# Performance work log

Hardware: AMD Instinct MI355X
Metric: run time of the kernel (lower is better)

Reference implementation:

```python
import jax, jax.numpy as jnp
import numpy as np

B, N, E, ENT, D, H, L = 64, 2048, 32768, 100000, 256, 256, 512


def setup_inputs() -> dict:
    key = jax.random.key(0)
    ks = jax.random.split(key, 12)
    return {
        "neighbors": jax.random.randint(ks[0], (B, N), 0, ENT),
        "adj_row": jax.random.randint(ks[1], (B, E), 0, N),
        "adj_col": jax.random.randint(ks[2], (B, E), 0, N),
        "adj_val": jax.random.uniform(ks[3], (B, E), dtype=jnp.float32),
        "emb_table": jax.random.normal(ks[4], (ENT, D), dtype=jnp.float32),
        "W1": jax.random.normal(ks[5], (D, H), dtype=jnp.float32) * (1.0 / np.sqrt(H)),
        "b1": jax.random.normal(ks[6], (H,), dtype=jnp.float32) * 0.01,
        "W2": jax.random.normal(ks[7], (H, H), dtype=jnp.float32) * (1.0 / np.sqrt(H)),
        "b2": jax.random.normal(ks[8], (H,), dtype=jnp.float32) * 0.01,
        "fc1_w": jax.random.normal(ks[9], (H, H), dtype=jnp.float32) * (1.0 / np.sqrt(H)),
        "fc1_b": jax.random.normal(ks[10], (H,), dtype=jnp.float32) * 0.01,
        "cur_len": L,
    }


def _gcn_layer(x, W, b, adj_row, adj_col, adj_val):
    # x: [B,N,din] -> support: [B,N,dout]
    support = jnp.einsum("bnd,dh->bnh", x, W)
    # sparse adj @ support: gather columns, scale by edge value, scatter-add to rows
    gathered = jnp.take_along_axis(support, adj_col[:, :, None], axis=1)  # [B,E,h]
    weighted = gathered * adj_val[:, :, None]
    agg = jax.vmap(lambda r, g: jax.ops.segment_sum(g, r, num_segments=N))(adj_row, weighted)
    return agg + b


def reference(neighbors, adj_row, adj_col, adj_val, emb_table, W1, b1, W2, b2, fc1_w, fc1_b, cur_len):
    x = emb_table[neighbors]                                   # [B,N,D] embedding gather
    x = _gcn_layer(x, W1, b1, adj_row, adj_col, adj_val)       # GCN layer 1
    x = _gcn_layer(x, W2, b2, adj_row, adj_col, adj_val)       # GCN layer 2
    seq = x[:, :cur_len, :]                                    # keep cur_node prefix, padded to common L
    pooled = jnp.mean(seq, axis=1, keepdims=True)              # self.seq == 'mean'
    return jax.nn.relu(jnp.einsum("blh,ho->blo", pooled, fc1_w) + fc1_b)  # [B,1,H]
```

## Files before the change

kernel.cpp:

```cpp
#include <hip/hip_runtime.h>

#define B 64
#define N 2048
#define E 32768
#define D 256
#define H 256
#define CH 32
#define SEG 16
#define EPB (E / SEG)

__global__ __launch_bounds__(256) void edge_w_kernel(
    const int* __restrict__ adj_row, const int* __restrict__ adj_col,
    const float* __restrict__ adj_val, const int* __restrict__ cur_len,
    float* __restrict__ w_out, float* __restrict__ sw_out)
{
    __shared__ float wloc[N];
    __shared__ float sred[4];
    const int b = blockIdx.x, seg = blockIdx.y, tid = threadIdx.x;
    const int L = *cur_len;

    for (int i = tid; i < N; i += 256) wloc[i] = 0.f;
    __syncthreads();

    const int base = b * E + seg * EPB;
    float svp = 0.f;
    for (int e = tid; e < EPB; e += 256) {
        int r = adj_row[base + e];
        if (r < L) {
            float v = adj_val[base + e];
            atomicAdd(&wloc[adj_col[base + e]], v);
            svp += v;
        }
    }
    __syncthreads();

    for (int i = tid; i < N; i += 256) {
        float v = wloc[i];
        if (v != 0.f) atomicAdd(&w_out[(size_t)b * N + i], v);
    }
    for (int off = 32; off; off >>= 1) svp += __shfl_down(svp, off, 64);
    if ((tid & 63) == 0) sred[tid >> 6] = svp;
    __syncthreads();
    if (tid == 0) atomicAdd(&sw_out[b], sred[0] + sred[1] + sred[2] + sred[3]);
}

__global__ __launch_bounds__(256) void edge_z_kernel(
    const int* __restrict__ adj_row, const int* __restrict__ adj_col,
    const float* __restrict__ adj_val, const float* __restrict__ w,
    float* __restrict__ z_out)
{
    __shared__ float zloc[N];
    const int b = blockIdx.x, seg = blockIdx.y, tid = threadIdx.x;

    for (int i = tid; i < N; i += 256) zloc[i] = 0.f;
    __syncthreads();

    const int base = b * E + seg * EPB;
    const float* wb = w + (size_t)b * N;
    for (int e = tid; e < EPB; e += 256) {
        float wv = wb[adj_row[base + e]];
        if (wv != 0.f) atomicAdd(&zloc[adj_col[base + e]], wv * adj_val[base + e]);
    }
    __syncthreads();

    for (int i = tid; i < N; i += 256) {
        float v = zloc[i];
        if (v != 0.f) atomicAdd(&z_out[(size_t)b * N + i], v);
    }
}

__global__ __launch_bounds__(256) void gather_kernel(
    const int* __restrict__ neighbors, const float* __restrict__ emb,
    const float* __restrict__ z, float* __restrict__ u_part)
{
    const int b = blockIdx.x, chunk = blockIdx.y, tid = threadIdx.x;
    const int lane = tid & 63, rg = tid >> 6;
    const float4* __restrict__ emb4 = (const float4*)emb;
    float4 acc = make_float4(0.f, 0.f, 0.f, 0.f);

    const int n0 = chunk * (N / CH);
    #pragma unroll 4
    for (int i = 0; i < (N / CH) / 4; ++i) {
        const int n = n0 + 4 * i + rg;
        const float zv = z[(size_t)b * N + n];
        const long idx = (long)neighbors[(size_t)b * N + n];
        const float4 v = emb4[idx * (D / 4) + lane];
        acc.x += zv * v.x; acc.y += zv * v.y;
        acc.z += zv * v.z; acc.w += zv * v.w;
    }

    __shared__ float4 red[256];
    red[tid] = acc;
    __syncthreads();
    if (tid < 64) {
        float4 a = red[tid], bb = red[tid + 64], c = red[tid + 128], d = red[tid + 192];
        float4 s = make_float4(a.x + bb.x + c.x + d.x, a.y + bb.y + c.y + d.y,
                               a.z + bb.z + c.z + d.z, a.w + bb.w + c.w + d.w);
        ((float4*)u_part)[((size_t)b * CH + chunk) * (D / 4) + tid] = s;
    }
}

__global__ __launch_bounds__(256) void head_kernel(
    const float* __restrict__ u_part, const float* __restrict__ sw,
    const float* __restrict__ W1, const float* __restrict__ b1,
    const float* __restrict__ W2, const float* __restrict__ b2,
    const float* __restrict__ fc1_w, const float* __restrict__ fc1_b,
    const int* __restrict__ cur_len, float* __restrict__ out)
{
    const int b = blockIdx.x, t = threadIdx.x;
    __shared__ float su[D];
    __shared__ float sy[H];
    __shared__ float sp[H];

    float uacc = 0.f;
    #pragma unroll 8
    for (int c = 0; c < CH; ++c) uacc += u_part[((size_t)b * CH + c) * D + t];
    su[t] = uacc;
    __syncthreads();

    float acc = sw[b] * b1[t];
    #pragma unroll 8
    for (int d = 0; d < D; ++d) acc += su[d] * W1[d * H + t];
    sy[t] = acc;
    __syncthreads();

    const float invL = 1.f / (float)(*cur_len);
    acc = 0.f;
    #pragma unroll 8
    for (int k = 0; k < H; ++k) acc += sy[k] * W2[k * H + t];
    sp[t] = acc * invL + b2[t];
    __syncthreads();

    acc = fc1_b[t];
    #pragma unroll 8
    for (int k = 0; k < H; ++k) acc += sp[k] * fc1_w[k * H + t];
    out[b * H + t] = fmaxf(acc, 0.f);
}

extern "C" void kernel_launch(void* const* d_in, const int* in_sizes, int n_in,
                              void* d_out, int out_size, void* d_ws, size_t ws_size,
                              hipStream_t stream) {
    const int*   neighbors = (const int*)  d_in[0];
    const int*   adj_row   = (const int*)  d_in[1];
    const int*   adj_col   = (const int*)  d_in[2];
    const float* adj_val   = (const float*)d_in[3];
    const float* emb_table = (const float*)d_in[4];
    const float* W1        = (const float*)d_in[5];
    const float* b1        = (const float*)d_in[6];
    const float* W2        = (const float*)d_in[7];
    const float* b2        = (const float*)d_in[8];
    const float* fc1_w     = (const float*)d_in[9];
    const float* fc1_b     = (const float*)d_in[10];
    const int*   cur_len   = (const int*)  d_in[11];
    float*       out       = (float*)d_out;

    float* w_ws  = (float*)d_ws;
    float* z_ws  = w_ws + (size_t)B * N;
    float* sw_ws = z_ws + (size_t)B * N;
    float* u_ws  = sw_ws + 64;

    hipMemsetAsync(d_ws, 0, ((size_t)2 * B * N + 64) * sizeof(float), stream);

    edge_w_kernel<<<dim3(B, SEG), 256, 0, stream>>>(adj_row, adj_col, adj_val,
                                                    cur_len, w_ws, sw_ws);
    edge_z_kernel<<<dim3(B, SEG), 256, 0, stream>>>(adj_row, adj_col, adj_val,
                                                    w_ws, z_ws);
    gather_kernel<<<dim3(B, CH), 256, 0, stream>>>(neighbors, emb_table, z_ws, u_ws);
    head_kernel<<<B, 256, 0, stream>>>(u_ws, sw_ws, W1, b1, W2, b2,
                                       fc1_w, fc1_b, cur_len, out);
}
```

Baseline: 275.2 us.

## Widen edge kernels to 512 threads, split-K head kernel, dual accumulators in gather

The edge kernels now use 8 segments of 512 threads with fully unrolled edge loops instead of 16 segments of 256. This halves the shared-to-global flush atomics and exposes more independent loads per thread. The head kernel uses 1024 threads and splits each 256-wide reduction into four partial sums combined through shared memory, so each thread's serial matvec chain is a quarter as long. The gather kernel alternates between two accumulators to break the FMA dependency chain. Risks include fewer blocks per batch reducing parallelism and more barriers in the head kernel.

```diff
diff --git a/kernel.cpp b/kernel.cpp
--- a/kernel.cpp
+++ b/kernel.cpp
@@ -6,45 +6,53 @@
 #define D 256
 #define H 256
 #define CH 32
-#define SEG 16
+#define SEG 8
 #define EPB (E / SEG)
 
-__global__ __launch_bounds__(256) void edge_w_kernel(
+__global__ __launch_bounds__(512) void edge_w_kernel(
     const int* __restrict__ adj_row, const int* __restrict__ adj_col,
     const float* __restrict__ adj_val, const int* __restrict__ cur_len,
     float* __restrict__ w_out, float* __restrict__ sw_out)
 {
     __shared__ float wloc[N];
-    __shared__ float sred[4];
+    __shared__ float sred[8];
     const int b = blockIdx.x, seg = blockIdx.y, tid = threadIdx.x;
     const int L = *cur_len;
 
-    for (int i = tid; i < N; i += 256) wloc[i] = 0.f;
+    for (int i = tid; i < N; i += 512) wloc[i] = 0.f;
     __syncthreads();
 
     const int base = b * E + seg * EPB;
     float svp = 0.f;
-    for (int e = tid; e < EPB; e += 256) {
-        int r = adj_row[base + e];
+    #pragma unroll
+    for (int k = 0; k < EPB / 512; ++k) {
+        const int e = base + tid + k * 512;
+        const int r = adj_row[e];
         if (r < L) {
-            float v = adj_val[base + e];
-            atomicAdd(&wloc[adj_col[base + e]], v);
+            const float v = adj_val[e];
+            atomicAdd(&wloc[adj_col[e]], v);
             svp += v;
         }
     }
     __syncthreads();
 
-    for (int i = tid; i < N; i += 256) {
-        float v = wloc[i];
+    #pragma unroll
+    for (int i = tid; i < N; i += 512) {
+        const float v = wloc[i];
         if (v != 0.f) atomicAdd(&w_out[(size_t)b * N + i], v);
     }
     for (int off = 32; off; off >>= 1) svp += __shfl_down(svp, off, 64);
     if ((tid & 63) == 0) sred[tid >> 6] = svp;
     __syncthreads();
-    if (tid == 0) atomicAdd(&sw_out[b], sred[0] + sred[1] + sred[2] + sred[3]);
-}
-
-__global__ __launch_bounds__(256) void edge_z_kernel(
+    if (tid == 0) {
+        float s = 0.f;
+        #pragma unroll
+        for (int i = 0; i < 8; ++i) s += sred[i];
+        atomicAdd(&sw_out[b], s);
+    }
+}
+
+__global__ __launch_bounds__(512) void edge_z_kernel(
     const int* __restrict__ adj_row, const int* __restrict__ adj_col,
     const float* __restrict__ adj_val, const float* __restrict__ w,
     float* __restrict__ z_out)
@@ -52,19 +60,22 @@
     __shared__ float zloc[N];
     const int b = blockIdx.x, seg = blockIdx.y, tid = threadIdx.x;
 
-    for (int i = tid; i < N; i += 256) zloc[i] = 0.f;
+    for (int i = tid; i < N; i += 512) zloc[i] = 0.f;
     __syncthreads();
 
     const int base = b * E + seg * EPB;
-    const float* wb = w + (size_t)b * N;
-    for (int e = tid; e < EPB; e += 256) {
-        float wv = wb[adj_row[base + e]];
-        if (wv != 0.f) atomicAdd(&zloc[adj_col[base + e]], wv * adj_val[base + e]);
-    }
-    __syncthreads();
-
-    for (int i = tid; i < N; i += 256) {
-        float v = zloc[i];
+    const float* __restrict__ wb = w + (size_t)b * N;
+    #pragma unroll
+    for (int k = 0; k < EPB / 512; ++k) {
+        const int e = base + tid + k * 512;
+        const float wv = wb[adj_row[e]];
+        if (wv != 0.f) atomicAdd(&zloc[adj_col[e]], wv * adj_val[e]);
+    }
+    __syncthreads();
+
+    #pragma unroll
+    for (int i = tid; i < N; i += 512) {
+        const float v = zloc[i];
         if (v != 0.f) atomicAdd(&z_out[(size_t)b * N + i], v);
     }
 }
@@ -76,18 +87,26 @@
     const int b = blockIdx.x, chunk = blockIdx.y, tid = threadIdx.x;
     const int lane = tid & 63, rg = tid >> 6;
     const float4* __restrict__ emb4 = (const float4*)emb;
-    float4 acc = make_float4(0.f, 0.f, 0.f, 0.f);
+    float4 acc0 = make_float4(0.f, 0.f, 0.f, 0.f);
+    float4 acc1 = make_float4(0.f, 0.f, 0.f, 0.f);
 
     const int n0 = chunk * (N / CH);
-    #pragma unroll 4
+    #pragma unroll 8
     for (int i = 0; i < (N / CH) / 4; ++i) {
         const int n = n0 + 4 * i + rg;
         const float zv = z[(size_t)b * N + n];
         const long idx = (long)neighbors[(size_t)b * N + n];
         const float4 v = emb4[idx * (D / 4) + lane];
-        acc.x += zv * v.x; acc.y += zv * v.y;
-        acc.z += zv * v.z; acc.w += zv * v.w;
-    }
+        if (i & 1) {
+            acc1.x += zv * v.x; acc1.y += zv * v.y;
+            acc1.z += zv * v.z; acc1.w += zv * v.w;
+        } else {
+            acc0.x += zv * v.x; acc0.y += zv * v.y;
+            acc0.z += zv * v.z; acc0.w += zv * v.w;
+        }
+    }
+    float4 acc = make_float4(acc0.x + acc1.x, acc0.y + acc1.y,
+                             acc0.z + acc1.z, acc0.w + acc1.w);
 
     __shared__ float4 red[256];
     red[tid] = acc;
@@ -100,41 +119,66 @@
     }
 }
 
-__global__ __launch_bounds__(256) void head_kernel(
+__global__ __launch_bounds__(1024) void head_kernel(
     const float* __restrict__ u_part, const float* __restrict__ sw,
     const float* __restrict__ W1, const float* __restrict__ b1,
     const float* __restrict__ W2, const float* __restrict__ b2,
     const float* __restrict__ fc1_w, const float* __restrict__ fc1_b,
     const int* __restrict__ cur_len, float* __restrict__ out)
 {
-    const int b = blockIdx.x, t = threadIdx.x;
+    const int b = blockIdx.x;
+    const int t = threadIdx.x & 255;
+    const int s = threadIdx.x >> 8;
+    __shared__ float red[4][256];
     __shared__ float su[D];
     __shared__ float sy[H];
     __shared__ float sp[H];
 
-    float uacc = 0.f;
-    #pragma unroll 8
-    for (int c = 0; c < CH; ++c) uacc += u_part[((size_t)b * CH + c) * D + t];
-    su[t] = uacc;
-    __syncthreads();
-
-    float acc = sw[b] * b1[t];
-    #pragma unroll 8
-    for (int d = 0; d < D; ++d) acc += su[d] * W1[d * H + t];
-    sy[t] = acc;
+    float part = 0.f;
+    #pragma unroll
+    for (int c = 0; c < 8; ++c)
+        part += u_part[((size_t)b * CH + s * 8 + c) * D + t];
+    red[s][t] = part;
+    __syncthreads();
+    if (s == 0) su[t] = red[0][t] + red[1][t] + red[2][t] + red[3][t];
+    __syncthreads();
+
+    part = 0.f;
+    #pragma unroll 8
+    for (int k = 0; k < 64; ++k) {
+        const int d = s * 64 + k;
+        part += su[d] * W1[d * H + t];
+    }
+    red[s][t] = part;
+    __syncthreads();
+    if (s == 0) sy[t] = red[0][t] + red[1][t] + red[2][t] + red[3][t] + sw[b] * b1[t];
     __syncthreads();
 
     const float invL = 1.f / (float)(*cur_len);
-    acc = 0.f;
-    #pragma unroll 8
-    for (int k = 0; k < H; ++k) acc += sy[k] * W2[k * H + t];
-    sp[t] = acc * invL + b2[t];
-    __syncthreads();
-
-    acc = fc1_b[t];
-    #pragma unroll 8
-    for (int k = 0; k < H; ++k) acc += sp[k] * fc1_w[k * H + t];
-    out[b * H + t] = fmaxf(acc, 0.f);
+    part = 0.f;
+    #pragma unroll 8
+    for (int k = 0; k < 64; ++k) {
+        const int d = s * 64 + k;
+        part += sy[d] * W2[d * H + t];
+    }
+    red[s][t] = part;
+    __syncthreads();
+    if (s == 0)
+        sp[t] = (red[0][t] + red[1][t] + red[2][t] + red[3][t]) * invL + b2[t];
+    __syncthreads();
+
+    part = 0.f;
+    #pragma unroll 8
+    for (int k = 0; k < 64; ++k) {
+        const int d = s * 64 + k;
+        part += sp[d] * fc1_w[d * H + t];
+    }
+    red[s][t] = part;
+    __syncthreads();
+    if (s == 0) {
+        const float v = red[0][t] + red[1][t] + red[2][t] + red[3][t] + fc1_b[t];
+        out[(size_t)b * H + t] = fmaxf(v, 0.f);
+    }
 }
 
 extern "C" void kernel_launch(void* const* d_in, const int* in_sizes, int n_in,
@@ -161,11 +205,11 @@
 
     hipMemsetAsync(d_ws, 0, ((size_t)2 * B * N + 64) * sizeof(float), stream);
 
-    edge_w_kernel<<<dim3(B, SEG), 256, 0, stream>>>(adj_row, adj_col, adj_val,
+    edge_w_kernel<<<dim3(B, SEG), 512, 0, stream>>>(adj_row, adj_col, adj_val,
                                                     cur_len, w_ws, sw_ws);
-    edge_z_kernel<<<dim3(B, SEG), 256, 0, stream>>>(adj_row, adj_col, adj_val,
+    edge_z_kernel<<<dim3(B, SEG), 512, 0, stream>>>(adj_row, adj_col, adj_val,
                                                     w_ws, z_ws);
     gather_kernel<<<dim3(B, CH), 256, 0, stream>>>(neighbors, emb_table, z_ws, u_ws);
-    head_kernel<<<B, 256, 0, stream>>>(u_ws, sw_ws, W1, b1, W2, b2,
-                                       fc1_w, fc1_b, cur_len, out);
-}
+    head_kernel<<<B, 1024, 0, stream>>>(u_ws, sw_ws, W1, b1, W2, b2,
+                                        fc1_w, fc1_b, cur_len, out);
+}
```

Measured after the change: 231.9 us. 1.19x faster.
